# Kernel optimization log

Hardware: AMD Instinct MI355X
Metric: run time of the kernel (lower is better)

## Reference

```python
import jax, jax.numpy as jnp
import numpy as np

B, S, D = 2, 2048, 1024
H, DH = 16, 64
INNER = H * DH  # 1024
FF = 4 * D
WINDOW = 128
EPS = 1e-5
SCALE = DH ** -0.5


def setup_inputs() -> dict:
    key = jax.random.key(0)
    ks = jax.random.split(key, 8)
    s = lambda fan_in: 1.0 / np.sqrt(fan_in)
    return {
        "x": jax.random.normal(ks[0], (B, S, D), dtype=jnp.float32),
        "ln1_g": jnp.ones((D,), jnp.float32),
        "ln1_b": jnp.zeros((D,), jnp.float32),
        "w_qkv": jax.random.uniform(ks[1], (3 * INNER, D), jnp.float32, -s(D), s(D)),
        "w_out": jax.random.uniform(ks[2], (D, INNER), jnp.float32, -s(INNER), s(INNER)),
        "b_out": jnp.zeros((D,), jnp.float32),
        "ln2_g": jnp.ones((D,), jnp.float32),
        "ln2_b": jnp.zeros((D,), jnp.float32),
        "w_ff1": jax.random.uniform(ks[3], (FF, D), jnp.float32, -s(D), s(D)),
        "b_ff1": jnp.zeros((FF,), jnp.float32),
        "w_ff2": jax.random.uniform(ks[4], (D, FF), jnp.float32, -s(FF), s(FF)),
        "b_ff2": jnp.zeros((D,), jnp.float32),
    }


def _layernorm(x, g, b):
    mu = jnp.mean(x, axis=-1, keepdims=True)
    var = jnp.mean(jnp.square(x - mu), axis=-1, keepdims=True)
    return (x - mu) * jax.lax.rsqrt(var + EPS) * g + b


def reference(x, ln1_g, ln1_b, w_qkv, w_out, b_out, ln2_g, ln2_b, w_ff1, b_ff1, w_ff2, b_ff2):
    # --- attention block ---
    residual = x
    h = _layernorm(x, ln1_g, ln1_b)
    qkv = h @ w_qkv.T                             # [B, S, 3*INNER]
    q, k, v = jnp.split(qkv, 3, axis=-1)
    reshape_heads = lambda t: t.reshape(B, S, H, DH).transpose(0, 2, 1, 3)  # [B,H,S,DH]
    q, k, v = map(reshape_heads, (q, k, v))
    q = q * SCALE
    scores = jnp.einsum("bhqd,bhkd->bhqk", q, k)  # dense [B,H,S,S]
    # local sparse pattern: attend iff |i-j| <= window_size
    idx = jnp.arange(S)
    local_mask = jnp.abs(idx[:, None] - idx[None, :]) <= WINDOW  # [S,S] bool
    scores = jnp.where(local_mask[None, None], scores, -jnp.inf)
    attn = jax.nn.softmax(scores, axis=-1)
    attn = jnp.nan_to_num(attn, nan=0.0)
    out = jnp.einsum("bhqk,bhkd->bhqd", attn, v)  # [B,H,S,DH]
    out = out.transpose(0, 2, 1, 3).reshape(B, S, INNER)
    out = out @ w_out.T + b_out                   # dropout inactive (eval)
    x = residual + out
    # --- FFN block ---
    residual = x
    h = _layernorm(x, ln2_g, ln2_b)
    h = jax.nn.gelu(h @ w_ff1.T + b_ff1, approximate=False)
    h = h @ w_ff2.T + b_ff2
    return residual + h
```

## Files before the change

### kernel.cpp

```cpp
#include <hip/hip_runtime.h>
#include <stdint.h>

#define SEQ    2048
#define NB     2
#define DMODEL 1024
#define NHEAD  16
#define HDIM   64
#define FFDIM  4096
#define WIN    128
#define MTOK   (NB*SEQ)

typedef short short8 __attribute__((ext_vector_type(8)));
typedef float f32x4  __attribute__((ext_vector_type(4)));

__device__ __forceinline__ float bf2f(uint16_t h){ return __uint_as_float(((uint32_t)h) << 16); }
__device__ __forceinline__ uint16_t f2bf(float f){
  uint32_t u = __float_as_uint(f);
  u += 0x7fffu + ((u >> 16) & 1u);
  return (uint16_t)(u >> 16);
}
__device__ __forceinline__ int sw4(int r){ return (r ^ (r >> 2)) & 3; }

__device__ __forceinline__ void gl_lds16(const void* g, void* l) {
  __builtin_amdgcn_global_load_lds((const __attribute__((address_space(1))) void*)g,
                                   (__attribute__((address_space(3))) void*)l, 16, 0, 0);
}

__global__ __launch_bounds__(256) void cvt4_kernel(
    const float* __restrict__ s0, const float* __restrict__ s1,
    const float* __restrict__ s2, const float* __restrict__ s3,
    uint16_t* __restrict__ d0, uint16_t* __restrict__ d1,
    uint16_t* __restrict__ d2, uint16_t* __restrict__ d3)
{
  size_t i = (size_t)blockIdx.x * 256 + threadIdx.x;
  const float* s; uint16_t* d; size_t off;
  if      (i <  768*1024) { s = s0; d = d0; off = i; }
  else if (i < 1024*1024) { s = s1; d = d1; off = i -  768*1024; }
  else if (i < 2048*1024) { s = s2; d = d2; off = i - 1024*1024; }
  else                    { s = s3; d = d3; off = i - 2048*1024; }
  const float4 v = ((const float4*)s)[off];
  uint2 o;
  o.x = (uint32_t)f2bf(v.x) | ((uint32_t)f2bf(v.y) << 16);
  o.y = (uint32_t)f2bf(v.z) | ((uint32_t)f2bf(v.w) << 16);
  ((uint2*)d)[off] = o;
}

__global__ __launch_bounds__(256) void ln_kernel(const float* __restrict__ x,
                                                 const float* __restrict__ g,
                                                 const float* __restrict__ b,
                                                 uint16_t* __restrict__ y)
{
  const int row = blockIdx.x;
  const int t = threadIdx.x;
  const float4 v = ((const float4*)(x + (size_t)row * DMODEL))[t];
  float s1 = v.x + v.y + v.z + v.w;
  float s2 = v.x*v.x + v.y*v.y + v.z*v.z + v.w*v.w;
  #pragma unroll
  for (int off = 32; off; off >>= 1) { s1 += __shfl_xor(s1, off, 64); s2 += __shfl_xor(s2, off, 64); }
  __shared__ float red[8];
  const int w = t >> 6;
  if ((t & 63) == 0) { red[w] = s1; red[4+w] = s2; }
  __syncthreads();
  s1 = red[0]+red[1]+red[2]+red[3];
  s2 = red[4]+red[5]+red[6]+red[7];
  const float mu = s1 * (1.0f/DMODEL);
  const float var = s2 * (1.0f/DMODEL) - mu*mu;
  const float rs = rsqrtf(var + 1e-5f);
  const float4 gv = ((const float4*)g)[t];
  const float4 bv = ((const float4*)b)[t];
  const float o0 = (v.x-mu)*rs*gv.x + bv.x;
  const float o1 = (v.y-mu)*rs*gv.y + bv.y;
  const float o2 = (v.z-mu)*rs*gv.z + bv.z;
  const float o3 = (v.w-mu)*rs*gv.w + bv.w;
  uint2 o;
  o.x = (uint32_t)f2bf(o0) | ((uint32_t)f2bf(o1) << 16);
  o.y = (uint32_t)f2bf(o2) | ((uint32_t)f2bf(o3) << 16);
  ((uint2*)(y + (size_t)row * DMODEL))[t] = o;
}

template<int EPI, int OUT32>
__global__ __launch_bounds__(256) void gemm_bt(
    const uint16_t* __restrict__ A, const uint16_t* __restrict__ Bm,
    const float* __restrict__ bias, const float* __restrict__ res,
    void* __restrict__ Cv, int M, int N, int K)
{
  __shared__ __align__(16) uint16_t As[128*32];
  __shared__ __align__(16) uint16_t Bs[128*32];
  const int t = threadIdx.x;
  const int l = t & 63;
  const int w = t >> 6;
  const int row0 = blockIdx.y * 128;
  const int col0 = blockIdx.x * 128;
  const int wm = (w >> 1) * 64, wn = (w & 1) * 64;

  f32x4 acc[4][4];
  #pragma unroll
  for (int i = 0; i < 4; ++i)
    #pragma unroll
    for (int j = 0; j < 4; ++j)
      #pragma unroll
      for (int e = 0; e < 4; ++e) acc[i][j][e] = 0.0f;

  const int sr = t >> 2, ss = t & 3;
  const int sg = ss ^ sw4(sr);
  const uint16_t* aG = A  + (size_t)(row0 + sr) * K + sg * 8;
  const uint16_t* bG = Bm + (size_t)(col0 + sr) * K + sg * 8;
  char* aL = (char*)As + t * 16;
  char* bL = (char*)Bs + t * 16;
  const int mrow = l & 15;
  const int kq = l >> 4;
  const int slot = kq ^ sw4(mrow);

  for (int k0 = 0; k0 < K; k0 += 32) {
    gl_lds16(aG + k0,                   aL);
    gl_lds16(aG + k0 + (size_t)64 * K,  aL + 4096);
    gl_lds16(bG + k0,                   bL);
    gl_lds16(bG + k0 + (size_t)64 * K,  bL + 4096);
    __syncthreads();
    short8 af[4], bfr[4];
    #pragma unroll
    for (int mi = 0; mi < 4; ++mi)
      af[mi] = *(const short8*)((const char*)As + (wm + mi*16 + mrow) * 64 + slot * 16);
    #pragma unroll
    for (int ni = 0; ni < 4; ++ni)
      bfr[ni] = *(const short8*)((const char*)Bs + (wn + ni*16 + mrow) * 64 + slot * 16);
    #pragma unroll
    for (int mi = 0; mi < 4; ++mi)
      #pragma unroll
      for (int ni = 0; ni < 4; ++ni)
        acc[mi][ni] = __builtin_amdgcn_mfma_f32_16x16x32_bf16(af[mi], bfr[ni], acc[mi][ni], 0, 0, 0);
    __syncthreads();
  }

  const int crow = (l >> 4) * 4;
  float bv[4];
  #pragma unroll
  for (int ni = 0; ni < 4; ++ni)
    bv[ni] = (EPI != 0) ? bias[col0 + wn + ni*16 + mrow] : 0.0f;
  #pragma unroll
  for (int mi = 0; mi < 4; ++mi) {
    #pragma unroll
    for (int r = 0; r < 4; ++r) {
      const int row = row0 + wm + mi*16 + crow + r;
      #pragma unroll
      for (int ni = 0; ni < 4; ++ni) {
        const int col = col0 + wn + ni*16 + mrow;
        float v = acc[mi][ni][r] + bv[ni];
        if (EPI == 1) v += res[(size_t)row * N + col];
        if (EPI == 2) v = 0.5f * v * (1.0f + erff(v * 0.70710678118654752f));
        if (OUT32) ((float*)Cv)[(size_t)row * N + col] = v;
        else       ((uint16_t*)Cv)[(size_t)row * N + col] = f2bf(v);
      }
    }
  }
}

template<int EPI, int OUT32>
__global__ __launch_bounds__(256) void gemm_bt64(
    const uint16_t* __restrict__ A, const uint16_t* __restrict__ Bm,
    const float* __restrict__ bias, const float* __restrict__ res,
    void* __restrict__ Cv, int M, int N, int K)
{
  __shared__ __align__(16) uint16_t As[128*32];
  __shared__ __align__(16) uint16_t Bs[64*32];
  const int t = threadIdx.x;
  const int l = t & 63;
  const int w = t >> 6;
  const int row0 = blockIdx.y * 128;
  const int col0 = blockIdx.x * 64;
  const int wm = (w >> 1) * 64, wn = (w & 1) * 32;

  f32x4 acc[4][2];
  #pragma unroll
  for (int i = 0; i < 4; ++i)
    #pragma unroll
    for (int j = 0; j < 2; ++j)
      #pragma unroll
      for (int e = 0; e < 4; ++e) acc[i][j][e] = 0.0f;

  const int sr = t >> 2, ss = t & 3;
  const int sg = ss ^ sw4(sr);
  const uint16_t* aG = A  + (size_t)(row0 + sr) * K + sg * 8;
  const uint16_t* bG = Bm + (size_t)(col0 + sr) * K + sg * 8;
  char* aL = (char*)As + t * 16;
  char* bL = (char*)Bs + t * 16;
  const int mrow = l & 15;
  const int kq = l >> 4;
  const int slot = kq ^ sw4(mrow);

  for (int k0 = 0; k0 < K; k0 += 32) {
    gl_lds16(aG + k0,                   aL);
    gl_lds16(aG + k0 + (size_t)64 * K,  aL + 4096);
    gl_lds16(bG + k0,                   bL);
    __syncthreads();
    short8 af[4], bfr[2];
    #pragma unroll
    for (int mi = 0; mi < 4; ++mi)
      af[mi] = *(const short8*)((const char*)As + (wm + mi*16 + mrow) * 64 + slot * 16);
    #pragma unroll
    for (int ni = 0; ni < 2; ++ni)
      bfr[ni] = *(const short8*)((const char*)Bs + (wn + ni*16 + mrow) * 64 + slot * 16);
    #pragma unroll
    for (int mi = 0; mi < 4; ++mi)
      #pragma unroll
      for (int ni = 0; ni < 2; ++ni)
        acc[mi][ni] = __builtin_amdgcn_mfma_f32_16x16x32_bf16(af[mi], bfr[ni], acc[mi][ni], 0, 0, 0);
    __syncthreads();
  }

  const int crow = (l >> 4) * 4;
  float bv[2];
  #pragma unroll
  for (int ni = 0; ni < 2; ++ni)
    bv[ni] = (EPI != 0) ? bias[col0 + wn + ni*16 + mrow] : 0.0f;
  #pragma unroll
  for (int mi = 0; mi < 4; ++mi) {
    #pragma unroll
    for (int r = 0; r < 4; ++r) {
      const int row = row0 + wm + mi*16 + crow + r;
      #pragma unroll
      for (int ni = 0; ni < 2; ++ni) {
        const int col = col0 + wn + ni*16 + mrow;
        float v = acc[mi][ni][r] + bv[ni];
        if (EPI == 1) v += res[(size_t)row * N + col];
        if (EPI == 2) v = 0.5f * v * (1.0f + erff(v * 0.70710678118654752f));
        if (OUT32) ((float*)Cv)[(size_t)row * N + col] = v;
        else       ((uint16_t*)Cv)[(size_t)row * N + col] = f2bf(v);
      }
    }
  }
}

#define TQ    32
#define NKT   18
#define NKP   (NKT*16)
#define KSTR  72
#define PSTR  296

__global__ __launch_bounds__(256) void attn_kernel(const uint16_t* __restrict__ qkv,
                                                   uint16_t* __restrict__ out)
{
  __shared__ uint16_t Qs[TQ * KSTR];
  __shared__ uint16_t Ps[TQ * PSTR];
  __shared__ uint16_t KV[NKP * KSTR];
  const int t = threadIdx.x, l = t & 63, w = t >> 6;
  const int b = blockIdx.z, hh = blockIdx.y, q0 = blockIdx.x * TQ;
  const int k0 = (q0 - WIN > 0) ? (q0 - WIN) : 0;
  const int kend_ = q0 + TQ + WIN;
  const int kend = (kend_ < SEQ) ? kend_ : SEQ;
  const int nk = kend - k0;

  {
    const int r = t >> 3, gg = t & 7;
    const uint4 qv = *(const uint4*)(qkv + (size_t)(b*SEQ + q0 + r) * 3072 + hh*64 + gg*8);
    *(uint4*)((char*)Qs + r*(KSTR*2) + gg*16) = qv;
    for (int j = r; j < NKP; j += 32) {
      uint4 kv; kv.x = 0; kv.y = 0; kv.z = 0; kv.w = 0;
      if (j < nk)
        kv = *(const uint4*)(qkv + (size_t)(b*SEQ + k0 + j) * 3072 + 1024 + hh*64 + gg*8);
      *(uint4*)((char*)KV + j*(KSTR*2) + gg*16) = kv;
    }
  }
  __syncthreads();

  if (w < 2) {
    const int rb = w * 16;
    const int mrow = l & 15, q4 = l >> 4;
    const short8 aq0 = *(const short8*)((const char*)Qs + (rb + mrow)*(KSTR*2) + q4*16);
    const short8 aq1 = *(const short8*)((const char*)Qs + (rb + mrow)*(KSTR*2) + 64 + q4*16);
    f32x4 cacc[NKT];
    #pragma unroll
    for (int ct = 0; ct < NKT; ++ct) {
      f32x4 c; c[0]=0.f; c[1]=0.f; c[2]=0.f; c[3]=0.f;
      const short8 b0 = *(const short8*)((const char*)KV + (ct*16 + mrow)*(KSTR*2) + q4*16);
      const short8 b1 = *(const short8*)((const char*)KV + (ct*16 + mrow)*(KSTR*2) + 64 + q4*16);
      c = __builtin_amdgcn_mfma_f32_16x16x32_bf16(aq0, b0, c, 0, 0, 0);
      c = __builtin_amdgcn_mfma_f32_16x16x32_bf16(aq1, b1, c, 0, 0, 0);
      cacc[ct] = c;
    }
    #pragma unroll
    for (int r = 0; r < 4; ++r) {
      const int iq = q0 + rb + q4*4 + r;
      float m = -1e30f;
      #pragma unroll
      for (int ct = 0; ct < NKT; ++ct) {
        const int jj = ct*16 + mrow;
        const int j = k0 + jj;
        const bool ok = (jj < nk) && (j >= iq - WIN) && (j <= iq + WIN);
        const float s = ok ? cacc[ct][r] * 0.125f : -1e30f;
        cacc[ct][r] = s;
        m = fmaxf(m, s);
      }
      m = fmaxf(m, __shfl_xor(m, 1, 64));
      m = fmaxf(m, __shfl_xor(m, 2, 64));
      m = fmaxf(m, __shfl_xor(m, 4, 64));
      m = fmaxf(m, __shfl_xor(m, 8, 64));
      float s = 0.f;
      #pragma unroll
      for (int ct = 0; ct < NKT; ++ct) {
        const float e = __expf(cacc[ct][r] - m);
        cacc[ct][r] = e;
        s += e;
      }
      s += __shfl_xor(s, 1, 64);
      s += __shfl_xor(s, 2, 64);
      s += __shfl_xor(s, 4, 64);
      s += __shfl_xor(s, 8, 64);
      const float rinv = 1.0f / s;
      #pragma unroll
      for (int ct = 0; ct < NKT; ++ct)
        Ps[(rb + q4*4 + r) * PSTR + ct*16 + mrow] = f2bf(cacc[ct][r] * rinv);
    }
  }
  __syncthreads();

  {
    uint16_t* Vt = KV;
    const int gg = t & 7;
    for (int j = t >> 3; j < NKP; j += 32) {
      if (j < nk) {
        const uint4 v = *(const uint4*)(qkv + (size_t)(b*SEQ + k0 + j) * 3072 + 2048 + hh*64 + gg*8);
        uint16_t e[8] = { (uint16_t)(v.x & 0xffff), (uint16_t)(v.x >> 16),
                          (uint16_t)(v.y & 0xffff), (uint16_t)(v.y >> 16),
                          (uint16_t)(v.z & 0xffff), (uint16_t)(v.z >> 16),
                          (uint16_t)(v.w & 0xffff), (uint16_t)(v.w >> 16) };
        #pragma unroll
        for (int dd = 0; dd < 8; ++dd) Vt[(gg*8 + dd) * PSTR + j] = e[dd];
      } else {
        #pragma unroll
        for (int dd = 0; dd < 8; ++dd) Vt[(gg*8 + dd) * PSTR + j] = 0;
      }
    }
  }
  __syncthreads();

  {
    const uint16_t* Vt = KV;
    const int mrow = l & 15, q4 = l >> 4;
    const int rt = w & 1, dt0 = (w >> 1) * 2;
    f32x4 o0, o1;
    #pragma unroll
    for (int e = 0; e < 4; ++e) { o0[e] = 0.f; o1[e] = 0.f; }
    #pragma unroll
    for (int ks = 0; ks < 9; ++ks) {
      const short8 a  = *(const short8*)((const char*)Ps + (rt*16 + mrow)*(PSTR*2) + ks*64 + q4*16);
      const short8 v0 = *(const short8*)((const char*)Vt + ((dt0  )*16 + mrow)*(PSTR*2) + ks*64 + q4*16);
      const short8 v1 = *(const short8*)((const char*)Vt + ((dt0+1)*16 + mrow)*(PSTR*2) + ks*64 + q4*16);
      o0 = __builtin_amdgcn_mfma_f32_16x16x32_bf16(a, v0, o0, 0, 0, 0);
      o1 = __builtin_amdgcn_mfma_f32_16x16x32_bf16(a, v1, o1, 0, 0, 0);
    }
    #pragma unroll
    for (int r = 0; r < 4; ++r) {
      const int iq = q0 + rt*16 + q4*4 + r;
      const size_t rowoff = (size_t)(b*SEQ + iq) * DMODEL + hh*64;
      out[rowoff + (dt0  )*16 + mrow] = f2bf(o0[r]);
      out[rowoff + (dt0+1)*16 + mrow] = f2bf(o1[r]);
    }
  }
}

extern "C" void kernel_launch(void* const* d_in, const int* in_sizes, int n_in,
                              void* d_out, int out_size, void* d_ws, size_t ws_size,
                              hipStream_t stream)
{
  const float* x    = (const float*)d_in[0];
  const float* ln1g = (const float*)d_in[1];
  const float* ln1b = (const float*)d_in[2];
  const float* wqkv = (const float*)d_in[3];
  const float* wout = (const float*)d_in[4];
  const float* bout = (const float*)d_in[5];
  const float* ln2g = (const float*)d_in[6];
  const float* ln2b = (const float*)d_in[7];
  const float* wff1 = (const float*)d_in[8];
  const float* bff1 = (const float*)d_in[9];
  const float* wff2 = (const float*)d_in[10];
  const float* bff2 = (const float*)d_in[11];
  float* out = (float*)d_out;

  char* ws = (char*)d_ws;
  const size_t MB = (size_t)1 << 20;
  uint16_t* Wqkv = (uint16_t*)(ws);
  uint16_t* Wout = (uint16_t*)(ws +  6*MB);
  uint16_t* Wff1 = (uint16_t*)(ws +  8*MB);
  uint16_t* Wff2 = (uint16_t*)(ws + 16*MB);
  uint16_t* QKV  = (uint16_t*)(ws + 24*MB);
  uint16_t* H1   = (uint16_t*)(ws + 48*MB);
  uint16_t* AT   = H1;
  float*    X2f  = (float*)   (ws + 56*MB);
  uint16_t* H2   = (uint16_t*)(ws + 72*MB);
  uint16_t* FF1  = QKV;

  cvt4_kernel<<<12288, 256, 0, stream>>>(wqkv, wout, wff1, wff2, Wqkv, Wout, Wff1, Wff2);
  ln_kernel<<<MTOK, 256, 0, stream>>>(x, ln1g, ln1b, H1);
  gemm_bt<0,0><<<dim3(3072/128, MTOK/128), 256, 0, stream>>>(H1, Wqkv, nullptr, nullptr, QKV, MTOK, 3072, DMODEL);
  attn_kernel<<<dim3(SEQ/TQ, NHEAD, NB), 256, 0, stream>>>(QKV, AT);
  gemm_bt64<1,1><<<dim3(DMODEL/64, MTOK/128), 256, 0, stream>>>(AT, Wout, bout, x, X2f, MTOK, DMODEL, DMODEL);
  ln_kernel<<<MTOK, 256, 0, stream>>>(X2f, ln2g, ln2b, H2);
  gemm_bt<2,0><<<dim3(FFDIM/128, MTOK/128), 256, 0, stream>>>(H2, Wff1, bff1, nullptr, FF1, MTOK, FFDIM, DMODEL);
  gemm_bt64<1,1><<<dim3(DMODEL/64, MTOK/128), 256, 0, stream>>>(FF1, Wff2, bff2, X2f, out, MTOK, DMODEL, FFDIM);
}
```

Before: 385.0 us.

## Split-K the out-projection and FF2 GEMMs, fuse reductions with residual and LN2

The out-projection GEMM is split 2-way over K and writes fp32 partials. A new combine kernel sums the partials, adds bias and residual, and applies LayerNorm2, replacing the separate ln_kernel. The FF2 GEMM is split 4-way over K with 128x128 tiles writing bf16 partials, and a combine kernel reduces them with bias and residual. This raises the number of workgroups for the narrow N=1024 GEMMs, which should help fill the GPU, at the cost of extra partial-buffer traffic and bf16 rounding of the FF2 partials, which may reduce accuracy.

```diff
diff --git a/kernel.cpp b/kernel.cpp
--- a/kernel.cpp
+++ b/kernel.cpp
@@ -68,21 +68,17 @@
   const float rs = rsqrtf(var + 1e-5f);
   const float4 gv = ((const float4*)g)[t];
   const float4 bv = ((const float4*)b)[t];
-  const float o0 = (v.x-mu)*rs*gv.x + bv.x;
-  const float o1 = (v.y-mu)*rs*gv.y + bv.y;
-  const float o2 = (v.z-mu)*rs*gv.z + bv.z;
-  const float o3 = (v.w-mu)*rs*gv.w + bv.w;
   uint2 o;
-  o.x = (uint32_t)f2bf(o0) | ((uint32_t)f2bf(o1) << 16);
-  o.y = (uint32_t)f2bf(o2) | ((uint32_t)f2bf(o3) << 16);
+  o.x = (uint32_t)f2bf((v.x-mu)*rs*gv.x + bv.x) | ((uint32_t)f2bf((v.y-mu)*rs*gv.y + bv.y) << 16);
+  o.y = (uint32_t)f2bf((v.z-mu)*rs*gv.z + bv.z) | ((uint32_t)f2bf((v.w-mu)*rs*gv.w + bv.w) << 16);
   ((uint2*)(y + (size_t)row * DMODEL))[t] = o;
 }
 
-template<int EPI, int OUT32>
+template<int EPI>
 __global__ __launch_bounds__(256) void gemm_bt(
     const uint16_t* __restrict__ A, const uint16_t* __restrict__ Bm,
-    const float* __restrict__ bias, const float* __restrict__ res,
-    void* __restrict__ Cv, int M, int N, int K)
+    const float* __restrict__ bias, uint16_t* __restrict__ C,
+    int M, int N, int K)
 {
   __shared__ __align__(16) uint16_t As[128*32];
   __shared__ __align__(16) uint16_t Bs[128*32];
@@ -108,8 +104,7 @@
   char* aL = (char*)As + t * 16;
   char* bL = (char*)Bs + t * 16;
   const int mrow = l & 15;
-  const int kq = l >> 4;
-  const int slot = kq ^ sw4(mrow);
+  const int slot = (l >> 4) ^ sw4(mrow);
 
   for (int k0 = 0; k0 < K; k0 += 32) {
     gl_lds16(aG + k0,                   aL);
@@ -146,20 +141,17 @@
       for (int ni = 0; ni < 4; ++ni) {
         const int col = col0 + wn + ni*16 + mrow;
         float v = acc[mi][ni][r] + bv[ni];
-        if (EPI == 1) v += res[(size_t)row * N + col];
         if (EPI == 2) v = 0.5f * v * (1.0f + erff(v * 0.70710678118654752f));
-        if (OUT32) ((float*)Cv)[(size_t)row * N + col] = v;
-        else       ((uint16_t*)Cv)[(size_t)row * N + col] = f2bf(v);
+        C[(size_t)row * N + col] = f2bf(v);
       }
     }
   }
 }
 
-template<int EPI, int OUT32>
-__global__ __launch_bounds__(256) void gemm_bt64(
+__global__ __launch_bounds__(256) void gemm_sk64(
     const uint16_t* __restrict__ A, const uint16_t* __restrict__ Bm,
-    const float* __restrict__ bias, const float* __restrict__ res,
-    void* __restrict__ Cv, int M, int N, int K)
+    float* __restrict__ P0, float* __restrict__ P1,
+    int M, int N, int K, int KS)
 {
   __shared__ __align__(16) uint16_t As[128*32];
   __shared__ __align__(16) uint16_t Bs[64*32];
@@ -168,6 +160,8 @@
   const int w = t >> 6;
   const int row0 = blockIdx.y * 128;
   const int col0 = blockIdx.x * 64;
+  const int kbase = blockIdx.z * KS;
+  float* P = blockIdx.z ? P1 : P0;
   const int wm = (w >> 1) * 64, wn = (w & 1) * 32;
 
   f32x4 acc[4][2];
@@ -180,15 +174,14 @@
 
   const int sr = t >> 2, ss = t & 3;
   const int sg = ss ^ sw4(sr);
-  const uint16_t* aG = A  + (size_t)(row0 + sr) * K + sg * 8;
-  const uint16_t* bG = Bm + (size_t)(col0 + sr) * K + sg * 8;
+  const uint16_t* aG = A  + (size_t)(row0 + sr) * K + kbase + sg * 8;
+  const uint16_t* bG = Bm + (size_t)(col0 + sr) * K + kbase + sg * 8;
   char* aL = (char*)As + t * 16;
   char* bL = (char*)Bs + t * 16;
   const int mrow = l & 15;
-  const int kq = l >> 4;
-  const int slot = kq ^ sw4(mrow);
-
-  for (int k0 = 0; k0 < K; k0 += 32) {
+  const int slot = (l >> 4) ^ sw4(mrow);
+
+  for (int k0 = 0; k0 < KS; k0 += 32) {
     gl_lds16(aG + k0,                   aL);
     gl_lds16(aG + k0 + (size_t)64 * K,  aL + 4096);
     gl_lds16(bG + k0,                   bL);
@@ -209,26 +202,150 @@
   }
 
   const int crow = (l >> 4) * 4;
-  float bv[2];
-  #pragma unroll
-  for (int ni = 0; ni < 2; ++ni)
-    bv[ni] = (EPI != 0) ? bias[col0 + wn + ni*16 + mrow] : 0.0f;
-  #pragma unroll
-  for (int mi = 0; mi < 4; ++mi) {
+  #pragma unroll
+  for (int mi = 0; mi < 4; ++mi)
     #pragma unroll
     for (int r = 0; r < 4; ++r) {
       const int row = row0 + wm + mi*16 + crow + r;
       #pragma unroll
-      for (int ni = 0; ni < 2; ++ni) {
-        const int col = col0 + wn + ni*16 + mrow;
-        float v = acc[mi][ni][r] + bv[ni];
-        if (EPI == 1) v += res[(size_t)row * N + col];
-        if (EPI == 2) v = 0.5f * v * (1.0f + erff(v * 0.70710678118654752f));
-        if (OUT32) ((float*)Cv)[(size_t)row * N + col] = v;
-        else       ((uint16_t*)Cv)[(size_t)row * N + col] = f2bf(v);
-      }
-    }
-  }
+      for (int ni = 0; ni < 2; ++ni)
+        P[(size_t)row * N + col0 + wn + ni*16 + mrow] = acc[mi][ni][r];
+    }
+}
+
+__global__ __launch_bounds__(256) void gemm_sk128(
+    const uint16_t* __restrict__ A, const uint16_t* __restrict__ Bm,
+    uint16_t* __restrict__ P0, uint16_t* __restrict__ P1,
+    uint16_t* __restrict__ P2, uint16_t* __restrict__ P3,
+    int M, int N, int K, int KS)
+{
+  __shared__ __align__(16) uint16_t As[128*32];
+  __shared__ __align__(16) uint16_t Bs[128*32];
+  const int t = threadIdx.x;
+  const int l = t & 63;
+  const int w = t >> 6;
+  const int row0 = blockIdx.y * 128;
+  const int col0 = blockIdx.x * 128;
+  const int z = blockIdx.z;
+  const int kbase = z * KS;
+  uint16_t* P = (z < 2) ? (z ? P1 : P0) : (z == 2 ? P2 : P3);
+  const int wm = (w >> 1) * 64, wn = (w & 1) * 64;
+
+  f32x4 acc[4][4];
+  #pragma unroll
+  for (int i = 0; i < 4; ++i)
+    #pragma unroll
+    for (int j = 0; j < 4; ++j)
+      #pragma unroll
+      for (int e = 0; e < 4; ++e) acc[i][j][e] = 0.0f;
+
+  const int sr = t >> 2, ss = t & 3;
+  const int sg = ss ^ sw4(sr);
+  const uint16_t* aG = A  + (size_t)(row0 + sr) * K + kbase + sg * 8;
+  const uint16_t* bG = Bm + (size_t)(col0 + sr) * K + kbase + sg * 8;
+  char* aL = (char*)As + t * 16;
+  char* bL = (char*)Bs + t * 16;
+  const int mrow = l & 15;
+  const int slot = (l >> 4) ^ sw4(mrow);
+
+  for (int k0 = 0; k0 < KS; k0 += 32) {
+    gl_lds16(aG + k0,                   aL);
+    gl_lds16(aG + k0 + (size_t)64 * K,  aL + 4096);
+    gl_lds16(bG + k0,                   bL);
+    gl_lds16(bG + k0 + (size_t)64 * K,  bL + 4096);
+    __syncthreads();
+    short8 af[4], bfr[4];
+    #pragma unroll
+    for (int mi = 0; mi < 4; ++mi)
+      af[mi] = *(const short8*)((const char*)As + (wm + mi*16 + mrow) * 64 + slot * 16);
+    #pragma unroll
+    for (int ni = 0; ni < 4; ++ni)
+      bfr[ni] = *(const short8*)((const char*)Bs + (wn + ni*16 + mrow) * 64 + slot * 16);
+    #pragma unroll
+    for (int mi = 0; mi < 4; ++mi)
+      #pragma unroll
+      for (int ni = 0; ni < 4; ++ni)
+        acc[mi][ni] = __builtin_amdgcn_mfma_f32_16x16x32_bf16(af[mi], bfr[ni], acc[mi][ni], 0, 0, 0);
+    __syncthreads();
+  }
+
+  const int crow = (l >> 4) * 4;
+  #pragma unroll
+  for (int mi = 0; mi < 4; ++mi)
+    #pragma unroll
+    for (int r = 0; r < 4; ++r) {
+      const int row = row0 + wm + mi*16 + crow + r;
+      #pragma unroll
+      for (int ni = 0; ni < 4; ++ni)
+        P[(size_t)row * N + col0 + wn + ni*16 + mrow] = f2bf(acc[mi][ni][r]);
+    }
+}
+
+__global__ __launch_bounds__(256) void combine_ln2_kernel(
+    const float* __restrict__ p0, const float* __restrict__ p1,
+    const float* __restrict__ x,  const float* __restrict__ bout,
+    const float* __restrict__ g,  const float* __restrict__ b,
+    float* __restrict__ X2f, uint16_t* __restrict__ H2)
+{
+  const int row = blockIdx.x;
+  const int t = threadIdx.x;
+  const size_t off = (size_t)row * (DMODEL/4) + t;
+  const float4 a0 = ((const float4*)p0)[off];
+  const float4 a1 = ((const float4*)p1)[off];
+  const float4 xv = ((const float4*)x)[off];
+  const float4 bo = ((const float4*)bout)[t];
+  float4 v;
+  v.x = a0.x + a1.x + xv.x + bo.x;
+  v.y = a0.y + a1.y + xv.y + bo.y;
+  v.z = a0.z + a1.z + xv.z + bo.z;
+  v.w = a0.w + a1.w + xv.w + bo.w;
+  ((float4*)X2f)[off] = v;
+  float s1 = v.x + v.y + v.z + v.w;
+  float s2 = v.x*v.x + v.y*v.y + v.z*v.z + v.w*v.w;
+  #pragma unroll
+  for (int o = 32; o; o >>= 1) { s1 += __shfl_xor(s1, o, 64); s2 += __shfl_xor(s2, o, 64); }
+  __shared__ float red[8];
+  const int w = t >> 6;
+  if ((t & 63) == 0) { red[w] = s1; red[4+w] = s2; }
+  __syncthreads();
+  s1 = red[0]+red[1]+red[2]+red[3];
+  s2 = red[4]+red[5]+red[6]+red[7];
+  const float mu = s1 * (1.0f/DMODEL);
+  const float var = s2 * (1.0f/DMODEL) - mu*mu;
+  const float rs = rsqrtf(var + 1e-5f);
+  const float4 gv = ((const float4*)g)[t];
+  const float4 bv = ((const float4*)b)[t];
+  uint2 o;
+  o.x = (uint32_t)f2bf((v.x-mu)*rs*gv.x + bv.x) | ((uint32_t)f2bf((v.y-mu)*rs*gv.y + bv.y) << 16);
+  o.y = (uint32_t)f2bf((v.z-mu)*rs*gv.z + bv.z) | ((uint32_t)f2bf((v.w-mu)*rs*gv.w + bv.w) << 16);
+  ((uint2*)(H2 + (size_t)row * DMODEL))[t] = o;
+}
+
+__global__ __launch_bounds__(256) void combine_ff2_kernel(
+    const uint16_t* __restrict__ p0, const uint16_t* __restrict__ p1,
+    const uint16_t* __restrict__ p2, const uint16_t* __restrict__ p3,
+    const float* __restrict__ bff2, const float* __restrict__ X2f,
+    float* __restrict__ out)
+{
+  const int row = blockIdx.x;
+  const int t = threadIdx.x;
+  const size_t eoff = (size_t)row * DMODEL + t * 4;
+  const uint2 u0 = *(const uint2*)(p0 + eoff);
+  const uint2 u1 = *(const uint2*)(p1 + eoff);
+  const uint2 u2 = *(const uint2*)(p2 + eoff);
+  const uint2 u3 = *(const uint2*)(p3 + eoff);
+  const float4 xv = ((const float4*)X2f)[(size_t)row * (DMODEL/4) + t];
+  const float4 bo = ((const float4*)bff2)[t];
+  float4 v;
+  v.x = bf2f((uint16_t)(u0.x & 0xffff)) + bf2f((uint16_t)(u1.x & 0xffff))
+      + bf2f((uint16_t)(u2.x & 0xffff)) + bf2f((uint16_t)(u3.x & 0xffff)) + bo.x + xv.x;
+  v.y = bf2f((uint16_t)(u0.x >> 16)) + bf2f((uint16_t)(u1.x >> 16))
+      + bf2f((uint16_t)(u2.x >> 16)) + bf2f((uint16_t)(u3.x >> 16)) + bo.y + xv.y;
+  v.z = bf2f((uint16_t)(u0.y & 0xffff)) + bf2f((uint16_t)(u1.y & 0xffff))
+      + bf2f((uint16_t)(u2.y & 0xffff)) + bf2f((uint16_t)(u3.y & 0xffff)) + bo.z + xv.z;
+  v.w = bf2f((uint16_t)(u0.y >> 16)) + bf2f((uint16_t)(u1.y >> 16))
+      + bf2f((uint16_t)(u2.y >> 16)) + bf2f((uint16_t)(u3.y >> 16)) + bo.w + xv.w;
+  ((float4*)out)[(size_t)row * (DMODEL/4) + t] = v;
 }
 
 #define TQ    32
@@ -388,14 +505,21 @@
   uint16_t* AT   = H1;
   float*    X2f  = (float*)   (ws + 56*MB);
   uint16_t* H2   = (uint16_t*)(ws + 72*MB);
-  uint16_t* FF1  = QKV;
+  float*    OP0  = (float*)   (ws + 24*MB);
+  float*    OP1  = (float*)   (ws + 80*MB);
+  uint16_t* FF1  = (uint16_t*)(ws + 24*MB);
+  uint16_t* FP0  = (uint16_t*)(ws);
+  uint16_t* FP1  = (uint16_t*)(ws +  8*MB);
+  uint16_t* FP2  = (uint16_t*)(ws + 72*MB);
+  uint16_t* FP3  = (uint16_t*)(ws + 80*MB);
 
   cvt4_kernel<<<12288, 256, 0, stream>>>(wqkv, wout, wff1, wff2, Wqkv, Wout, Wff1, Wff2);
   ln_kernel<<<MTOK, 256, 0, stream>>>(x, ln1g, ln1b, H1);
-  gemm_bt<0,0><<<dim3(3072/128, MTOK/128), 256, 0, stream>>>(H1, Wqkv, nullptr, nullptr, QKV, MTOK, 3072, DMODEL);
+  gemm_bt<0><<<dim3(3072/128, MTOK/128), 256, 0, stream>>>(H1, Wqkv, nullptr, QKV, MTOK, 3072, DMODEL);
   attn_kernel<<<dim3(SEQ/TQ, NHEAD, NB), 256, 0, stream>>>(QKV, AT);
-  gemm_bt64<1,1><<<dim3(DMODEL/64, MTOK/128), 256, 0, stream>>>(AT, Wout, bout, x, X2f, MTOK, DMODEL, DMODEL);
-  ln_kernel<<<MTOK, 256, 0, stream>>>(X2f, ln2g, ln2b, H2);
-  gemm_bt<2,0><<<dim3(FFDIM/128, MTOK/128), 256, 0, stream>>>(H2, Wff1, bff1, nullptr, FF1, MTOK, FFDIM, DMODEL);
-  gemm_bt64<1,1><<<dim3(DMODEL/64, MTOK/128), 256, 0, stream>>>(FF1, Wff2, bff2, X2f, out, MTOK, DMODEL, FFDIM);
-}
+  gemm_sk64<<<dim3(DMODEL/64, MTOK/128, 2), 256, 0, stream>>>(AT, Wout, OP0, OP1, MTOK, DMODEL, DMODEL, DMODEL/2);
+  combine_ln2_kernel<<<MTOK, 256, 0, stream>>>(OP0, OP1, x, bout, ln2g, ln2b, X2f, H2);
+  gemm_bt<2><<<dim3(FFDIM/128, MTOK/128), 256, 0, stream>>>(H2, Wff1, bff1, FF1, MTOK, FFDIM, DMODEL);
+  gemm_sk128<<<dim3(DMODEL/128, MTOK/128, 4), 256, 0, stream>>>(FF1, Wff2, FP0, FP1, FP2, FP3, MTOK, DMODEL, FFDIM, FFDIM/4);
+  combine_ff2_kernel<<<MTOK, 256, 0, stream>>>(FP0, FP1, FP2, FP3, bff2, X2f, out);
+}
```

After: 394.5 us. +2.5%, slower.
